# Optimization experiments

Hardware: AMD Instinct MI355X
Metric: run time of the kernel (lower is better)

## Reference

```python
import jax, jax.numpy as jnp
import numpy as np

HIDDEN = 256   # HIDDEN_NUM
INPUT = 4      # fixed input_size
B, T = 128, 512


def _lstm_dir(xs, wi, wh, bi, bh):
    """Single-direction LSTM scan. xs: [T,B,D]; wi: [4H,D]; wh: [4H,H]; bi,bh: [4H].
    PyTorch gate order: i, f, g, o. Returns hidden states [T,B,H]."""
    Tn, Bn, _ = xs.shape
    Hn = wh.shape[1]
    # precompute input contribution for all timesteps (tiny D -> one big GEMM)
    gx = jnp.einsum('tbd,gd->tbg', xs, wi) + bi + bh  # [T,B,4H]

    def step(carry, g):
        h, c = carry
        g = g + h @ wh.T
        i, f, gg, o = jnp.split(g, 4, axis=-1)
        c = jax.nn.sigmoid(f) * c + jax.nn.sigmoid(i) * jnp.tanh(gg)
        h = jax.nn.sigmoid(o) * jnp.tanh(c)
        return (h, c), h

    init = (jnp.zeros((Bn, Hn), xs.dtype), jnp.zeros((Bn, Hn), xs.dtype))
    _, hs = jax.lax.scan(step, init, gx)
    return hs


def _lstm_bidir(xs, w_ih, w_hh, b_ih, b_hh):
    """xs: [T,B,D]; weights stacked over direction: w_ih [2,4H,D] etc. -> [T,B,2H]."""
    fwd = _lstm_dir(xs, w_ih[0], w_hh[0], b_ih[0], b_hh[0])
    bwd = _lstm_dir(xs[::-1], w_ih[1], w_hh[1], b_ih[1], b_hh[1])[::-1]
    return jnp.concatenate([fwd, bwd], axis=-1)


def setup_inputs() -> dict:
    key = jax.random.key(0)
    ks = jax.random.split(key, 12)
    k = 1.0 / np.sqrt(HIDDEN)
    u = lambda kk, shape: jax.random.uniform(kk, shape, jnp.float32, -k, k)
    H4 = 4 * HIDDEN
    return {
        'x': jax.random.normal(ks[0], (B, T, INPUT), jnp.float32),
        # layer 0 (input size 4), stacked [fwd, bwd]
        'w_ih0': u(ks[1], (2, H4, INPUT)),
        'w_hh0': u(ks[2], (2, H4, HIDDEN)),
        'b_ih0': u(ks[3], (2, H4)),
        'b_hh0': u(ks[4], (2, H4)),
        # layer 1 (input size 2H from bidirectional layer 0)
        'w_ih1': u(ks[5], (2, H4, 2 * HIDDEN)),
        'w_hh1': u(ks[6], (2, H4, HIDDEN)),
        'b_ih1': u(ks[7], (2, H4)),
        'b_hh1': u(ks[8], (2, H4)),
        # final linear: HIDDEN*2 -> 2
        'fc_w': u(ks[9], (2, 2 * HIDDEN)),
        'fc_b': u(ks[10], (2,)),
    }


def reference(x, w_ih0, w_hh0, b_ih0, b_hh0, w_ih1, w_hh1, b_ih1, b_hh1, fc_w, fc_b):
    xs = jnp.transpose(x, (1, 0, 2))                 # [T,B,4] (seq-major like torch)
    h0 = _lstm_bidir(xs, w_ih0, w_hh0, b_ih0, b_hh0)  # [T,B,2H]
    h1 = _lstm_bidir(h0, w_ih1, w_hh1, b_ih1, b_hh1)  # [T,B,2H]
    pooled = jnp.mean(h1, axis=0)                     # [B,2H]
    return pooled @ fc_w.T + fc_b                     # [B,2]
```

## Files before the change

### kernel.cpp

```cpp
#include <hip/hip_runtime.h>
#include <hip/hip_bf16.h>


typedef __bf16 bf16;
typedef __bf16 bf16x8 __attribute__((ext_vector_type(8)));
typedef float  f32x4  __attribute__((ext_vector_type(4)));
typedef unsigned int u32;
typedef unsigned long long u64;
typedef u64 u64x2 __attribute__((ext_vector_type(2)));

#define T_SEQ 512
#define BATCH 128
#define HID   256

#define H0_BYTES   67239936ULL
#define H1_BYTES   262144ULL
#define POOL_BYTES 262144ULL
#define FL0_OFF    (H0_BYTES + H1_BYTES + POOL_BYTES)
#define FL1_OFF    (FL0_OFF + 4096ULL)

#define MFMA16(a, b, c) __builtin_amdgcn_mfma_f32_16x16x32_bf16((a), (b), (c), 0, 0, 0)
#define AL(p)     __hip_atomic_load((p), __ATOMIC_RELAXED, __HIP_MEMORY_SCOPE_AGENT)
#define AS(p, v)  __hip_atomic_store((p), (v), __ATOMIC_RELAXED, __HIP_MEMORY_SCOPE_AGENT)

__device__ __forceinline__ float fsig(float v) {
    return __builtin_amdgcn_rcpf(1.0f + __expf(-v));
}
__device__ __forceinline__ float ftanh(float v) {
    float a = fabsf(v);
    float e = __expf(-2.0f * a);
    float r = (1.0f - e) * __builtin_amdgcn_rcpf(1.0f + e);
    return v < 0.0f ? -r : r;
}

__global__ void k_init(unsigned int* ws_u, int* flags0, int* flags1) {
    const int t = blockIdx.x * 256 + threadIdx.x;
    ws_u[t] = 0u;
    ws_u[(size_t)513 * 16384 + t] = 0u;
    unsigned int* h1u = ws_u + (H0_BYTES / 4);
    h1u[t] = 0u;
    h1u[32768 + t] = 0u;
    if (t < 1024) flags0[t] = 0;
    if (t < 2048) flags1[t] = 0;
}

__global__ __launch_bounds__(256, 1) void k_l0(
    const float* __restrict__ x, const float* __restrict__ wih,
    const float* __restrict__ whh, const float* __restrict__ bih,
    const float* __restrict__ bhh, bf16* __restrict__ h0,
    int* __restrict__ flags)
{
    __shared__ __align__(16) bf16 Hs[64][20];

    const int blk = blockIdx.x;
    const int dir = blk >> 5, bh = (blk >> 4) & 1, g = blk & 15;
    const int tid = threadIdx.x, wave = tid >> 6, lane = tid & 63;
    const int l15 = lane & 15, q = lane >> 4;
    const int j = g * 16 + l15;

    bf16x8 Bf[4][8];
#pragma unroll
    for (int tg = 0; tg < 4; ++tg) {
        const float* wr = whh + ((size_t)(dir * 1024 + tg * 256 + j)) * 256 + q * 8;
#pragma unroll
        for (int kt = 0; kt < 8; ++kt) {
            f32x4 aa = *(const f32x4*)(wr + kt * 32);
            f32x4 bb = *(const f32x4*)(wr + kt * 32 + 4);
            bf16x8 f;
            f[0] = (bf16)aa[0]; f[1] = (bf16)aa[1]; f[2] = (bf16)aa[2]; f[3] = (bf16)aa[3];
            f[4] = (bf16)bb[0]; f[5] = (bf16)bb[1]; f[6] = (bf16)bb[2]; f[7] = (bf16)bb[3];
            Bf[tg][kt] = f;
        }
    }
    float biasg[4], wx[4][4];
#pragma unroll
    for (int tg = 0; tg < 4; ++tg) {
        const int n = dir * 1024 + tg * 256 + j;
        biasg[tg] = bih[n] + bhh[n];
#pragma unroll
        for (int d2 = 0; d2 < 4; ++d2) wx[tg][d2] = wih[(size_t)n * 4 + d2];
    }

    float c4[4] = {0.f, 0.f, 0.f, 0.f};
    const int arow  = bh * 64 + wave * 16 + l15;
    const int lrow0 = wave * 16 + q * 4;
    const int mrow0 = bh * 64 + lrow0;
    const int srow = tid >> 2, scg = (tid & 3) * 4;
    int* fgrp = flags + (dir * 2 + bh) * 256;
    int budget = 30000000;

#pragma unroll 1
    for (int s = 1; s <= T_SEQ; ++s) {
        const int t_in = dir ? (T_SEQ - s) : (s - 1);

        f32x4 xv[4];
#pragma unroll
        for (int r = 0; r < 4; ++r)
            xv[r] = *(const f32x4*)(x + ((size_t)(mrow0 + r) * T_SEQ + t_in) * 4);
        f32x4 acc[4];
#pragma unroll
        for (int tg = 0; tg < 4; ++tg) {
#pragma unroll
            for (int r = 0; r < 4; ++r) {
                acc[tg][r] = biasg[tg] + xv[r][0] * wx[tg][0] + xv[r][1] * wx[tg][1]
                                       + xv[r][2] * wx[tg][2] + xv[r][3] * wx[tg][3];
            }
        }

        if (lane < 16) {
            const int need = s - 1;
            while (AL(fgrp + lane * 16) < need) {
                if (--budget < 0) break;
            }
        }
        asm volatile("" ::: "memory");

        const u64* hsrc = (const u64*)(h0 + ((size_t)(dir * 513 + (s - 1)) * BATCH + arow) * HID)
                          + q * 2;
        u64 av[16];
#pragma unroll
        for (int kt = 0; kt < 8; ++kt) {
            av[2 * kt]     = AL(hsrc + kt * 8);
            av[2 * kt + 1] = AL(hsrc + kt * 8 + 1);
        }
#pragma unroll
        for (int kt = 0; kt < 8; ++kt) {
            u64x2 t2; t2[0] = av[2 * kt]; t2[1] = av[2 * kt + 1];
            const bf16x8 A = __builtin_bit_cast(bf16x8, t2);
            acc[0] = MFMA16(A, Bf[0][kt], acc[0]);
            acc[1] = MFMA16(A, Bf[1][kt], acc[1]);
            acc[2] = MFMA16(A, Bf[2][kt], acc[2]);
            acc[3] = MFMA16(A, Bf[3][kt], acc[3]);
        }

#pragma unroll
        for (int r = 0; r < 4; ++r) {
            const float iv = fsig(acc[0][r]);
            const float fv = fsig(acc[1][r]);
            const float gv = ftanh(acc[2][r]);
            const float ov = fsig(acc[3][r]);
            c4[r] = fv * c4[r] + iv * gv;
            const float hv = ov * ftanh(c4[r]);
            Hs[lrow0 + r][l15] = (bf16)hv;
        }
        __syncthreads();
        {
            const u64 hv8 = *(const u64*)&Hs[srow][scg];
            u64* dst = (u64*)(h0 + ((size_t)(dir * 513 + s) * BATCH + bh * 64 + srow) * HID
                              + g * 16 + scg);
            AS(dst, hv8);
        }
        __syncthreads();
        if (tid == 0) AS(fgrp + g * 16, s);
    }
}

__global__ __launch_bounds__(256, 1) void k_l1(
    const float* __restrict__ wih1, const float* __restrict__ whh1,
    const float* __restrict__ bih1, const float* __restrict__ bhh1,
    bf16* __restrict__ h0, bf16* __restrict__ h1,
    float* __restrict__ pooled, int* __restrict__ flags)
{
    __shared__ float Gs[4][32][17];
    __shared__ __align__(16) bf16 Hs[32][20];
    __shared__ __align__(16) bf16 As1[32][264];

    const int blk = blockIdx.x;
    const int dir = blk >> 6, bq = (blk >> 4) & 3, g = blk & 15;
    const int tid = threadIdx.x, wave = tid >> 6, lane = tid & 63;
    const int l15 = lane & 15, q = lane >> 4;
    const int n = dir * 1024 + wave * 256 + g * 16 + l15;

    bf16x8 Bf[24];
#pragma unroll
    for (int kt = 0; kt < 24; ++kt) {
        const int k = kt * 32 + q * 8;
        const float* src = (kt < 8) ? (whh1 + (size_t)n * 256 + k)
                                    : (wih1 + (size_t)n * 512 + (k - 256));
        f32x4 aa = *(const f32x4*)src;
        f32x4 bb = *(const f32x4*)(src + 4);
        bf16x8 f;
        f[0] = (bf16)aa[0]; f[1] = (bf16)aa[1]; f[2] = (bf16)aa[2]; f[3] = (bf16)aa[3];
        f[4] = (bf16)bb[0]; f[5] = (bf16)bb[1]; f[6] = (bf16)bb[2]; f[7] = (bf16)bb[3];
        Bf[kt] = f;
    }
    const float biasw = bih1[n] + bhh1[n];
    const int r0 = tid >> 4, colu = tid & 15;
    float cst[2] = {0.f, 0.f}, pool[2] = {0.f, 0.f};
    int* fgrp = flags + (dir * 4 + bq) * 256;
    int budget = 30000000;

#pragma unroll 1
    for (int s = 1; s <= T_SEQ; ++s) {
        const int slotf = dir ? (513 - s) : s;
        const int slotb = dir ? s : (513 - s);

        f32x4 acc0 = {biasw, biasw, biasw, biasw};
        f32x4 acc1 = acc0;
        const bf16* f0 = h0 + ((size_t)slotf * BATCH + bq * 32 + l15) * HID + q * 8;
        const bf16* b0 = h0 + ((size_t)(513 + slotb) * BATCH + bq * 32 + l15) * HID + q * 8;
#pragma unroll
        for (int kt = 0; kt < 8; ++kt) {
            const bf16x8 af0 = *(const bf16x8*)(f0 + kt * 32);
            const bf16x8 af1 = *(const bf16x8*)(f0 + 16 * HID + kt * 32);
            acc0 = MFMA16(af0, Bf[8 + kt], acc0);
            acc1 = MFMA16(af1, Bf[8 + kt], acc1);
        }
#pragma unroll
        for (int kt = 0; kt < 8; ++kt) {
            const bf16x8 ab0 = *(const bf16x8*)(b0 + kt * 32);
            const bf16x8 ab1 = *(const bf16x8*)(b0 + 16 * HID + kt * 32);
            acc0 = MFMA16(ab0, Bf[16 + kt], acc0);
            acc1 = MFMA16(ab1, Bf[16 + kt], acc1);
        }

        if (lane < 16) {
            const int need = s - 1;
            while (AL(fgrp + lane * 16) < need) {
                if (--budget < 0) break;
            }
        }
        asm volatile("" ::: "memory");

        {
            const u64* hb = (const u64*)(h1 + ((size_t)(dir * 2 + ((s - 1) & 1)) * BATCH
                                               + bq * 32) * HID);
#pragma unroll
            for (int i = 0; i < 4; ++i) {
                const int chunk = tid + 256 * i;
                const int row = chunk >> 5, cc = chunk & 31;
                const u64* src = hb + (size_t)row * 32 + cc;
                const u64 lo = AL(hb + (size_t)row * 64 + cc * 2);
                const u64 hi = AL(hb + (size_t)row * 64 + cc * 2 + 1);
                (void)src;
                u64x2 t2; t2[0] = lo; t2[1] = hi;
                *(bf16x8*)(&As1[row][cc * 8]) = __builtin_bit_cast(bf16x8, t2);
            }
        }
        __syncthreads();

#pragma unroll
        for (int kt = 0; kt < 8; ++kt) {
            const bf16x8 a0 = *(const bf16x8*)(&As1[l15][kt * 32 + q * 8]);
            const bf16x8 a1 = *(const bf16x8*)(&As1[16 + l15][kt * 32 + q * 8]);
            acc0 = MFMA16(a0, Bf[kt], acc0);
            acc1 = MFMA16(a1, Bf[kt], acc1);
        }

#pragma unroll
        for (int r = 0; r < 4; ++r) {
            Gs[wave][q * 4 + r][l15]      = acc0[r];
            Gs[wave][16 + q * 4 + r][l15] = acc1[r];
        }
        __syncthreads();

#pragma unroll
        for (int rr = 0; rr < 2; ++rr) {
            const int r = r0 + rr * 16;
            const float iv = fsig(Gs[0][r][colu]);
            const float fv = fsig(Gs[1][r][colu]);
            const float gv = ftanh(Gs[2][r][colu]);
            const float ov = fsig(Gs[3][r][colu]);
            cst[rr] = fv * cst[rr] + iv * gv;
            const float hv = ov * ftanh(cst[rr]);
            pool[rr] += hv;
            Hs[r][colu] = (bf16)hv;
        }
        __syncthreads();
        {
            const int lrow = tid >> 3, c2 = (tid & 7) * 2;
            const u32 hv4 = *(const u32*)&Hs[lrow][c2];
            u32* dst = (u32*)(h1 + ((size_t)(dir * 2 + (s & 1)) * BATCH + bq * 32 + lrow) * HID
                              + g * 16 + c2);
            AS(dst, hv4);
        }
        __syncthreads();
        if (tid == 0) AS(fgrp + g * 16, s);
    }
#pragma unroll
    for (int rr = 0; rr < 2; ++rr) {
        const int r = r0 + rr * 16;
        pooled[((size_t)dir * BATCH + bq * 32 + r) * HID + g * 16 + colu] =
            pool[rr] * (1.0f / 512.0f);
    }
}

__global__ void k_fc(const float* __restrict__ pooled, const float* __restrict__ fcw,
                     const float* __restrict__ fcb, float* __restrict__ out)
{
    const int b = blockIdx.x;
    const int lane = threadIdx.x;
    float s0 = 0.f, s1 = 0.f;
#pragma unroll
    for (int jj = 0; jj < 8; ++jj) {
        const int jx = lane + jj * 64;
        const float p = (jx < 256) ? pooled[(size_t)b * 256 + jx]
                                   : pooled[32768 + (size_t)b * 256 + (jx - 256)];
        s0 += p * fcw[jx];
        s1 += p * fcw[512 + jx];
    }
#pragma unroll
    for (int off = 32; off > 0; off >>= 1) {
        s0 += __shfl_down(s0, off);
        s1 += __shfl_down(s1, off);
    }
    if (lane == 0) {
        out[b * 2 + 0] = s0 + fcb[0];
        out[b * 2 + 1] = s1 + fcb[1];
    }
}

extern "C" void kernel_launch(void* const* d_in, const int* in_sizes, int n_in,
                              void* d_out, int out_size, void* d_ws, size_t ws_size,
                              hipStream_t stream)
{
    const float* x    = (const float*)d_in[0];
    const float* wih0 = (const float*)d_in[1];
    const float* whh0 = (const float*)d_in[2];
    const float* bih0 = (const float*)d_in[3];
    const float* bhh0 = (const float*)d_in[4];
    const float* wih1 = (const float*)d_in[5];
    const float* whh1 = (const float*)d_in[6];
    const float* bih1 = (const float*)d_in[7];
    const float* bhh1 = (const float*)d_in[8];
    const float* fcw  = (const float*)d_in[9];
    const float* fcb  = (const float*)d_in[10];
    float* out = (float*)d_out;

    char* ws = (char*)d_ws;
    bf16* h0      = (bf16*)ws;
    bf16* h1      = (bf16*)(ws + H0_BYTES);
    float* pooled = (float*)(ws + H0_BYTES + H1_BYTES);
    int* flags0   = (int*)(ws + FL0_OFF);
    int* flags1   = (int*)(ws + FL1_OFF);

    k_init<<<dim3(64), dim3(256), 0, stream>>>((unsigned int*)ws, flags0, flags1);
    k_l0<<<dim3(64), dim3(256), 0, stream>>>(x, wih0, whh0, bih0, bhh0, h0, flags0);
    k_l1<<<dim3(128), dim3(256), 0, stream>>>(wih1, whh1, bih1, bhh1, h0, h1, pooled, flags1);
    k_fc<<<dim3(128), dim3(64), 0, stream>>>(pooled, fcw, fcb, out);
}
```

Measured before the change: 4.816 ms.

## Split layer-0 LSTM by batch rows so each block owns full hidden state

```diff
diff --git a/kernel.cpp b/kernel.cpp
--- a/kernel.cpp
+++ b/kernel.cpp
@@ -14,10 +14,9 @@
 #define HID   256
 
 #define H0_BYTES   67239936ULL
-#define H1_BYTES   262144ULL
-#define POOL_BYTES 262144ULL
-#define FL0_OFF    (H0_BYTES + H1_BYTES + POOL_BYTES)
-#define FL1_OFF    (FL0_OFF + 4096ULL)
+#define H1_OFF     H0_BYTES
+#define POOL_OFF   (H1_OFF + 262144ULL)
+#define FL1_OFF    (POOL_OFF + 262144ULL + 4096ULL)
 
 #define MFMA16(a, b, c) __builtin_amdgcn_mfma_f32_16x16x32_bf16((a), (b), (c), 0, 0, 0)
 #define AL(p)     __hip_atomic_load((p), __ATOMIC_RELAXED, __HIP_MEMORY_SCOPE_AGENT)
@@ -32,62 +31,63 @@
     float r = (1.0f - e) * __builtin_amdgcn_rcpf(1.0f + e);
     return v < 0.0f ? -r : r;
 }
-
-__global__ void k_init(unsigned int* ws_u, int* flags0, int* flags1) {
+__device__ __forceinline__ bf16x8 cvt8(const float* p) {
+    f32x4 aa = *(const f32x4*)p;
+    f32x4 bb = *(const f32x4*)(p + 4);
+    bf16x8 f;
+    f[0] = (bf16)aa[0]; f[1] = (bf16)aa[1]; f[2] = (bf16)aa[2]; f[3] = (bf16)aa[3];
+    f[4] = (bf16)bb[0]; f[5] = (bf16)bb[1]; f[6] = (bf16)bb[2]; f[7] = (bf16)bb[3];
+    return f;
+}
+
+__global__ void k_init(unsigned int* ws_u, int* flags1) {
     const int t = blockIdx.x * 256 + threadIdx.x;
-    ws_u[t] = 0u;
-    ws_u[(size_t)513 * 16384 + t] = 0u;
-    unsigned int* h1u = ws_u + (H0_BYTES / 4);
+    unsigned int* h1u = ws_u + (H1_OFF / 4);
     h1u[t] = 0u;
     h1u[32768 + t] = 0u;
-    if (t < 1024) flags0[t] = 0;
     if (t < 2048) flags1[t] = 0;
 }
 
-__global__ __launch_bounds__(256, 1) void k_l0(
+__global__ __launch_bounds__(512, 2) void k_l0(
     const float* __restrict__ x, const float* __restrict__ wih,
     const float* __restrict__ whh, const float* __restrict__ bih,
-    const float* __restrict__ bhh, bf16* __restrict__ h0,
-    int* __restrict__ flags)
+    const float* __restrict__ bhh, bf16* __restrict__ h0)
 {
-    __shared__ __align__(16) bf16 Hs[64][20];
+    __shared__ __align__(16) bf16 LW[8][2][8][512];
+    __shared__ __align__(16) bf16 Hx[16][264];
+    __shared__ __align__(16) float WX[1024][4];
+    __shared__ float BS[1024];
 
     const int blk = blockIdx.x;
-    const int dir = blk >> 5, bh = (blk >> 4) & 1, g = blk & 15;
-    const int tid = threadIdx.x, wave = tid >> 6, lane = tid & 63;
+    const int dir = blk >> 3, rbase = (blk & 7) * 16;
+    const int tid = threadIdx.x, w = tid >> 6, lane = tid & 63;
     const int l15 = lane & 15, q = lane >> 4;
-    const int j = g * 16 + l15;
-
-    bf16x8 Bf[4][8];
-#pragma unroll
-    for (int tg = 0; tg < 4; ++tg) {
-        const float* wr = whh + ((size_t)(dir * 1024 + tg * 256 + j)) * 256 + q * 8;
-#pragma unroll
-        for (int kt = 0; kt < 8; ++kt) {
-            f32x4 aa = *(const f32x4*)(wr + kt * 32);
-            f32x4 bb = *(const f32x4*)(wr + kt * 32 + 4);
-            bf16x8 f;
-            f[0] = (bf16)aa[0]; f[1] = (bf16)aa[1]; f[2] = (bf16)aa[2]; f[3] = (bf16)aa[3];
-            f[4] = (bf16)bb[0]; f[5] = (bf16)bb[1]; f[6] = (bf16)bb[2]; f[7] = (bf16)bb[3];
-            Bf[tg][kt] = f;
-        }
-    }
-    float biasg[4], wx[4][4];
-#pragma unroll
-    for (int tg = 0; tg < 4; ++tg) {
-        const int n = dir * 1024 + tg * 256 + j;
-        biasg[tg] = bih[n] + bhh[n];
-#pragma unroll
-        for (int d2 = 0; d2 < 4; ++d2) wx[tg][d2] = wih[(size_t)n * 4 + d2];
-    }
-
-    float c4[4] = {0.f, 0.f, 0.f, 0.f};
-    const int arow  = bh * 64 + wave * 16 + l15;
-    const int lrow0 = wave * 16 + q * 4;
-    const int mrow0 = bh * 64 + lrow0;
-    const int srow = tid >> 2, scg = (tid & 3) * 4;
-    int* fgrp = flags + (dir * 2 + bh) * 256;
-    int budget = 30000000;
+
+    bf16x8 Bf[6][8];
+#pragma unroll
+    for (int nt = 0; nt < 6; ++nt) {
+        const int n = (nt >> 1) * 256 + w * 32 + (nt & 1) * 16 + l15;
+        const float* wr = whh + ((size_t)(dir * 1024 + n)) * 256 + q * 8;
+#pragma unroll
+        for (int kt = 0; kt < 8; ++kt) Bf[nt][kt] = cvt8(wr + kt * 32);
+    }
+#pragma unroll
+    for (int tt = 0; tt < 2; ++tt) {
+        const int n = 768 + w * 32 + tt * 16 + l15;
+        const float* wr = whh + ((size_t)(dir * 1024 + n)) * 256 + q * 8;
+#pragma unroll
+        for (int kt = 0; kt < 8; ++kt)
+            *(bf16x8*)&LW[w][tt][kt][lane * 8] = cvt8(wr + kt * 32);
+    }
+    for (int nn = tid; nn < 1024; nn += 512) {
+        const int n = dir * 1024 + nn;
+        *(f32x4*)&WX[nn][0] = *(const f32x4*)(wih + (size_t)n * 4);
+        BS[nn] = bih[n] + bhh[n];
+    }
+    for (int i2 = tid; i2 < 16 * 264 / 2; i2 += 512) ((u32*)Hx)[i2] = 0u;
+
+    float c4[2][4] = {{0.f, 0.f, 0.f, 0.f}, {0.f, 0.f, 0.f, 0.f}};
+    __syncthreads();
 
 #pragma unroll 1
     for (int s = 1; s <= T_SEQ; ++s) {
@@ -96,62 +96,56 @@
         f32x4 xv[4];
 #pragma unroll
         for (int r = 0; r < 4; ++r)
-            xv[r] = *(const f32x4*)(x + ((size_t)(mrow0 + r) * T_SEQ + t_in) * 4);
-        f32x4 acc[4];
-#pragma unroll
-        for (int tg = 0; tg < 4; ++tg) {
-#pragma unroll
-            for (int r = 0; r < 4; ++r) {
-                acc[tg][r] = biasg[tg] + xv[r][0] * wx[tg][0] + xv[r][1] * wx[tg][1]
-                                       + xv[r][2] * wx[tg][2] + xv[r][3] * wx[tg][3];
-            }
-        }
-
-        if (lane < 16) {
-            const int need = s - 1;
-            while (AL(fgrp + lane * 16) < need) {
-                if (--budget < 0) break;
-            }
-        }
-        asm volatile("" ::: "memory");
-
-        const u64* hsrc = (const u64*)(h0 + ((size_t)(dir * 513 + (s - 1)) * BATCH + arow) * HID)
-                          + q * 2;
-        u64 av[16];
+            xv[r] = *(const f32x4*)(x + ((size_t)(rbase + q * 4 + r) * T_SEQ + t_in) * 4);
+        f32x4 acc[8];
+#pragma unroll
+        for (int nt = 0; nt < 8; ++nt) {
+            const int n = (nt >> 1) * 256 + w * 32 + (nt & 1) * 16 + l15;
+            const f32x4 wx4 = *(const f32x4*)&WX[n][0];
+            const float bs = BS[n];
+#pragma unroll
+            for (int r = 0; r < 4; ++r)
+                acc[nt][r] = bs + xv[r][0] * wx4[0] + xv[r][1] * wx4[1]
+                                + xv[r][2] * wx4[2] + xv[r][3] * wx4[3];
+        }
+
 #pragma unroll
         for (int kt = 0; kt < 8; ++kt) {
-            av[2 * kt]     = AL(hsrc + kt * 8);
-            av[2 * kt + 1] = AL(hsrc + kt * 8 + 1);
-        }
-#pragma unroll
-        for (int kt = 0; kt < 8; ++kt) {
-            u64x2 t2; t2[0] = av[2 * kt]; t2[1] = av[2 * kt + 1];
-            const bf16x8 A = __builtin_bit_cast(bf16x8, t2);
+            const bf16x8 A  = *(const bf16x8*)&Hx[l15][kt * 32 + q * 8];
+            const bf16x8 b6 = *(const bf16x8*)&LW[w][0][kt][lane * 8];
+            const bf16x8 b7 = *(const bf16x8*)&LW[w][1][kt][lane * 8];
             acc[0] = MFMA16(A, Bf[0][kt], acc[0]);
             acc[1] = MFMA16(A, Bf[1][kt], acc[1]);
             acc[2] = MFMA16(A, Bf[2][kt], acc[2]);
             acc[3] = MFMA16(A, Bf[3][kt], acc[3]);
-        }
-
-#pragma unroll
-        for (int r = 0; r < 4; ++r) {
-            const float iv = fsig(acc[0][r]);
-            const float fv = fsig(acc[1][r]);
-            const float gv = ftanh(acc[2][r]);
-            const float ov = fsig(acc[3][r]);
-            c4[r] = fv * c4[r] + iv * gv;
-            const float hv = ov * ftanh(c4[r]);
-            Hs[lrow0 + r][l15] = (bf16)hv;
-        }
-        __syncthreads();
+            acc[4] = MFMA16(A, Bf[4][kt], acc[4]);
+            acc[5] = MFMA16(A, Bf[5][kt], acc[5]);
+            acc[6] = MFMA16(A, b6, acc[6]);
+            acc[7] = MFMA16(A, b7, acc[7]);
+        }
+        __syncthreads();
+
+#pragma unroll
+        for (int half = 0; half < 2; ++half) {
+            const int hcol = w * 32 + half * 16 + l15;
+#pragma unroll
+            for (int r = 0; r < 4; ++r) {
+                const float iv = fsig(acc[0 + half][r]);
+                const float fv = fsig(acc[2 + half][r]);
+                const float gv = ftanh(acc[4 + half][r]);
+                const float ov = fsig(acc[6 + half][r]);
+                c4[half][r] = fv * c4[half][r] + iv * gv;
+                const float hv = ov * ftanh(c4[half][r]);
+                Hx[q * 4 + r][hcol] = (bf16)hv;
+            }
+        }
+        __syncthreads();
+
         {
-            const u64 hv8 = *(const u64*)&Hs[srow][scg];
-            u64* dst = (u64*)(h0 + ((size_t)(dir * 513 + s) * BATCH + bh * 64 + srow) * HID
-                              + g * 16 + scg);
-            AS(dst, hv8);
-        }
-        __syncthreads();
-        if (tid == 0) AS(fgrp + g * 16, s);
+            const int row = tid >> 5, c8 = (tid & 31) * 8;
+            const bf16x8 hv = *(const bf16x8*)&Hx[row][c8];
+            *(bf16x8*)(h0 + ((size_t)(dir * 513 + s) * BATCH + rbase + row) * HID + c8) = hv;
+        }
     }
 }
 
@@ -177,12 +171,7 @@
         const int k = kt * 32 + q * 8;
         const float* src = (kt < 8) ? (whh1 + (size_t)n * 256 + k)
                                     : (wih1 + (size_t)n * 512 + (k - 256));
-        f32x4 aa = *(const f32x4*)src;
-        f32x4 bb = *(const f32x4*)(src + 4);
-        bf16x8 f;
-        f[0] = (bf16)aa[0]; f[1] = (bf16)aa[1]; f[2] = (bf16)aa[2]; f[3] = (bf16)aa[3];
-        f[4] = (bf16)bb[0]; f[5] = (bf16)bb[1]; f[6] = (bf16)bb[2]; f[7] = (bf16)bb[3];
-        Bf[kt] = f;
+        Bf[kt] = cvt8(src);
     }
     const float biasw = bih1[n] + bhh1[n];
     const int r0 = tid >> 4, colu = tid & 15;
@@ -229,22 +218,19 @@
             for (int i = 0; i < 4; ++i) {
                 const int chunk = tid + 256 * i;
                 const int row = chunk >> 5, cc = chunk & 31;
-                const u64* src = hb + (size_t)row * 32 + cc;
                 const u64 lo = AL(hb + (size_t)row * 64 + cc * 2);
                 const u64 hi = AL(hb + (size_t)row * 64 + cc * 2 + 1);
-                (void)src;
                 u64x2 t2; t2[0] = lo; t2[1] = hi;
                 *(bf16x8*)(&As1[row][cc * 8]) = __builtin_bit_cast(bf16x8, t2);
             }
-        }
-        __syncthreads();
-
-#pragma unroll
-        for (int kt = 0; kt < 8; ++kt) {
-            const bf16x8 a0 = *(const bf16x8*)(&As1[l15][kt * 32 + q * 8]);
-            const bf16x8 a1 = *(const bf16x8*)(&As1[16 + l15][kt * 32 + q * 8]);
-            acc0 = MFMA16(a0, Bf[kt], acc0);
-            acc1 = MFMA16(a1, Bf[kt], acc1);
+            __syncthreads();
+#pragma unroll
+            for (int kt = 0; kt < 8; ++kt) {
+                const bf16x8 a0 = *(const bf16x8*)(&As1[l15][kt * 32 + q * 8]);
+                const bf16x8 a1 = *(const bf16x8*)(&As1[16 + l15][kt * 32 + q * 8]);
+                acc0 = MFMA16(a0, Bf[kt], acc0);
+                acc1 = MFMA16(a1, Bf[kt], acc1);
+            }
         }
 
 #pragma unroll
@@ -329,13 +315,12 @@
 
     char* ws = (char*)d_ws;
     bf16* h0      = (bf16*)ws;
-    bf16* h1      = (bf16*)(ws + H0_BYTES);
-    float* pooled = (float*)(ws + H0_BYTES + H1_BYTES);
-    int* flags0   = (int*)(ws + FL0_OFF);
+    bf16* h1      = (bf16*)(ws + H1_OFF);
+    float* pooled = (float*)(ws + POOL_OFF);
     int* flags1   = (int*)(ws + FL1_OFF);
 
-    k_init<<<dim3(64), dim3(256), 0, stream>>>((unsigned int*)ws, flags0, flags1);
-    k_l0<<<dim3(64), dim3(256), 0, stream>>>(x, wih0, whh0, bih0, bhh0, h0, flags0);
+    k_init<<<dim3(64), dim3(256), 0, stream>>>((unsigned int*)ws, flags1);
+    k_l0<<<dim3(16), dim3(512), 0, stream>>>(x, wih0, whh0, bih0, bhh0, h0);
     k_l1<<<dim3(128), dim3(256), 0, stream>>>(wih1, whh1, bih1, bhh1, h0, h1, pooled, flags1);
     k_fc<<<dim3(128), dim3(64), 0, stream>>>(pooled, fcw, fcb, out);
 }
```

Result: slower. 4.988 ms (+3.6%).
